# Optimization experiments

Measured on AMD Instinct MI355X. Metric: run time of the kernel, lower is better.

The kernel has to match this reference:

```python
import jax, jax.numpy as jnp
import numpy as np

N_NODES = 50000
N_EDGES = 800000
D_IN = 128
D_HID = 128
D_OUT = 128


def setup_inputs() -> dict:
    key = jax.random.key(0)
    ks = jax.random.split(key, 12)
    features = jax.random.normal(ks[0], (N_NODES, D_IN), dtype=jnp.float32)
    src = jax.random.randint(ks[1], (N_EDGES,), 0, N_NODES, dtype=jnp.int32)
    dst = jax.random.randint(ks[2], (N_EDGES,), 0, N_NODES, dtype=jnp.int32)
    s_in = 1.0 / np.sqrt(D_IN)
    s_hid = 1.0 / np.sqrt(D_HID)
    W1 = jax.random.normal(ks[3], (D_IN, D_HID), dtype=jnp.float32) * s_in
    b1 = jnp.zeros((D_HID,), dtype=jnp.float32)
    W2 = jax.random.normal(ks[4], (D_HID, D_HID), dtype=jnp.float32) * s_hid
    b2 = jnp.zeros((D_HID,), dtype=jnp.float32)
    W3 = jax.random.normal(ks[5], (D_HID, D_OUT), dtype=jnp.float32) * s_hid
    b3 = jnp.zeros((D_OUT,), dtype=jnp.float32)
    policy_w = jax.random.normal(ks[6], (D_OUT, 1), dtype=jnp.float32) * s_hid
    policy_b = jnp.zeros((1,), dtype=jnp.float32)
    value_w = jax.random.normal(ks[7], (D_OUT, 1), dtype=jnp.float32) * s_hid
    value_b = jnp.zeros((1,), dtype=jnp.float32)
    return {
        "features": features, "src": src, "dst": dst,
        "W1": W1, "b1": b1, "W2": W2, "b2": b2, "W3": W3, "b3": b3,
        "policy_w": policy_w, "policy_b": policy_b,
        "value_w": value_w, "value_b": value_b,
    }


def _graph_conv(h, src, dst, deg_inv, W, b, act):
    # DGL GraphConv with norm='left': scale source features by 1/out_degree,
    # sum messages over incoming edges, then linear transform + bias (+ act).
    hn = h * deg_inv  # [N, d]
    agg = jax.ops.segment_sum(hn[src], dst, num_segments=N_NODES)  # SpMM: [N, d]
    out = agg @ W + b
    return jax.nn.relu(out) if act else out


def reference(features, src, dst, W1, b1, W2, b2, W3, b3,
              policy_w, policy_b, value_w, value_b):
    ones = jnp.ones((src.shape[0],), dtype=features.dtype)
    deg = jax.ops.segment_sum(ones, src, num_segments=N_NODES)  # out-degree
    deg_inv = (1.0 / jnp.clip(deg, 1.0))[:, None]  # [N, 1]

    h = _graph_conv(features, src, dst, deg_inv, W1, b1, act=True)
    h = _graph_conv(h, src, dst, deg_inv, W2, b2, act=True)
    h = _graph_conv(h, src, dst, deg_inv, W3, b3, act=False)  # last layer: no activation

    mN = jnp.mean(h, axis=0, keepdims=True)  # mean readout over nodes, [1, D_OUT]
    PI = h @ policy_w + policy_b  # [N, 1]
    V = mN @ value_w + value_b    # [1, 1]
    return PI, V
```

## Files before the change

kernel.cpp:

```cpp
#include <hip/hip_runtime.h>


#define N_NODES 50000
#define N_EDGES 800000
#define D 128
#define NSH 8
#define PROWS (N_NODES + 8)
#define PANEL ((size_t)PROWS * 16)
#define NC 64
#define CSZ (N_EDGES / NC)
#define NW (N_NODES / 2)
#define CS_CAP (N_EDGES + 8 * N_NODES)


__global__ __launch_bounds__(512) void k_hist3(const int* __restrict__ src, const int* __restrict__ dst,
                                               unsigned* __restrict__ ghd16, unsigned* __restrict__ ghs16) {
    __shared__ unsigned h[NW];
    const int arr = blockIdx.x & 1;
    const int c   = blockIdx.x >> 1;
    const int t = threadIdx.x;
    for (int i = t; i < NW; i += 512) h[i] = 0u;
    __syncthreads();
    const int* __restrict__ col = arr ? src : dst;
    const int e0 = c * CSZ, e1 = e0 + CSZ;
    for (int e = e0 + t; e < e1; e += 512) {
        int n = col[e];
        atomicAdd(&h[n >> 1], 1u << ((n & 1) << 4));
    }
    __syncthreads();
    unsigned* __restrict__ outp = (arr ? ghs16 : ghd16) + (size_t)c * NW;
    for (int i = t; i < NW; i += 512) outp[i] = h[i];
}

__global__ __launch_bounds__(256) void k_merge3(unsigned* __restrict__ ghd16, const unsigned* __restrict__ ghs16,
                                                int* __restrict__ rowcnt, int* __restrict__ rowtrue,
                                                float* __restrict__ dinv) {
    int w = blockIdx.x * 256 + threadIdx.x;
    if (w >= NW) return;
    unsigned runlo = 0, runhi = 0;
#pragma unroll
    for (int c = 0; c < NC; c++) {
        unsigned v = ghd16[(size_t)c * NW + w];
        ghd16[(size_t)c * NW + w] = runlo | (runhi << 16);
        runlo += v & 0xffffu; runhi += v >> 16;
    }
    rowtrue[2 * w]     = (int)runlo;
    rowtrue[2 * w + 1] = (int)runhi;
    rowcnt[2 * w]      = (int)((runlo + 7u) & ~7u);
    rowcnt[2 * w + 1]  = (int)((runhi + 7u) & ~7u);
    unsigned dlo = 0, dhi = 0;
#pragma unroll
    for (int c = 0; c < NC; c++) {
        unsigned v = ghs16[(size_t)c * NW + w];
        dlo += v & 0xffffu; dhi += v >> 16;
    }
    dinv[2 * w]     = 1.0f / (float)(dlo > 1u ? dlo : 1u);
    dinv[2 * w + 1] = 1.0f / (float)(dhi > 1u ? dhi : 1u);
}

__global__ __launch_bounds__(1024) void k_scan1(const int* __restrict__ cnt, int* __restrict__ excl,
                                                int* __restrict__ blocksum, int n) {
    __shared__ int wsum[16];
    int i = blockIdx.x * 1024 + threadIdx.x;
    int v = (i < n) ? cnt[i] : 0;
    int lane = threadIdx.x & 63, wid = threadIdx.x >> 6;
    int x = v;
#pragma unroll
    for (int off = 1; off < 64; off <<= 1) {
        int y = __shfl_up(x, off, 64);
        if (lane >= off) x += y;
    }
    if (lane == 63) wsum[wid] = x;
    __syncthreads();
    if (threadIdx.x == 0) {
        int run = 0;
        for (int w = 0; w < 16; w++) { int t = wsum[w]; wsum[w] = run; run += t; }
        blocksum[blockIdx.x] = run;
    }
    __syncthreads();
    if (i < n) excl[i] = (x - v) + wsum[wid];
}

__global__ void k_scan2(const int* __restrict__ blocksum, int* __restrict__ blockoff,
                        int* __restrict__ rowptr_last, int nblk) {
    if (threadIdx.x == 0) {
        int run = 0;
        for (int b = 0; b < nblk; b++) { int t = blocksum[b]; blockoff[b] = run; run += t; }
        rowptr_last[0] = run;
    }
}

__global__ __launch_bounds__(1024) void k_scan3(int* __restrict__ excl, const int* __restrict__ blockoff, int n) {
    int i = blockIdx.x * 1024 + threadIdx.x;
    if (i < n) excl[i] += blockoff[blockIdx.x];
}

__global__ __launch_bounds__(512) void k_fill3(const int* __restrict__ src, const int* __restrict__ dst,
                                               const int* __restrict__ rowptr, const unsigned* __restrict__ ghd16,
                                               unsigned short* __restrict__ cs16) {
    __shared__ unsigned cnt[NW];
    const int c = blockIdx.x;
    const int t = threadIdx.x;
    for (int i = t; i < NW; i += 512) cnt[i] = 0u;
    __syncthreads();
    const unsigned* __restrict__ basep = ghd16 + (size_t)c * NW;
    const int e0 = c * CSZ, e1 = e0 + CSZ;
    for (int e = e0 + t; e < e1; e += 512) {
        int d = dst[e];
        int sh = (d & 1) << 4;
        unsigned old = atomicAdd(&cnt[d >> 1], 1u << sh);
        int p = (int)((old >> sh) & 0xffffu);
        int base = (int)((basep[d >> 1] >> sh) & 0xffffu);
        cs16[rowptr[d] + base + p] = (unsigned short)src[e];
    }
}

__global__ __launch_bounds__(256) void k_pad(const int* __restrict__ rowptr, const int* __restrict__ rowtrue,
                                             unsigned short* __restrict__ cs16,
                                             float* __restrict__ bufA, float* __restrict__ bufB) {
    int n = blockIdx.x * 256 + threadIdx.x;
    if (n < N_NODES) {
        int e0 = rowptr[n] + rowtrue[n], e1 = rowptr[n + 1];
        for (int e = e0; e < e1; e++) cs16[e] = (unsigned short)N_NODES;
    }
    if (blockIdx.x == 0) {
        int t = threadIdx.x;
        float* b = (t & 128) ? bufB : bufA;
        int p = (t >> 4) & 7, cc = t & 15;
        b[(size_t)p * PANEL + (size_t)N_NODES * 16 + cc] = 0.f;
    }
}


__global__ __launch_bounds__(256) void k_panelize(const float* __restrict__ in, const float* __restrict__ dinv,
                                                  float* __restrict__ outp) {
    int tid = blockIdx.x * 256 + threadIdx.x;
    if (tid >= N_NODES * 32) return;
    int p = tid / (N_NODES * 4);
    int r = tid - p * (N_NODES * 4);
    int node = r >> 2, qq = r & 3;
    float w = dinv[node];
    float4 v = *reinterpret_cast<const float4*>(&in[(size_t)node * D + p * 16 + qq * 4]);
    v.x *= w; v.y *= w; v.z *= w; v.w *= w;
    *reinterpret_cast<float4*>(&outp[(size_t)p * PANEL + (size_t)node * 16 + qq * 4]) = v;
}


__global__ __launch_bounds__(256) void k_agg(const float* __restrict__ hp,
                                             const int* __restrict__ rp, const unsigned short* __restrict__ cs16,
                                             float* __restrict__ outp) {
    const int l4 = threadIdx.x & 3;
    const int grp = threadIdx.x >> 2;
    const int slice = blockIdx.x & (NSH - 1);
    const int node = (blockIdx.x >> 3) * 64 + grp;
    if (node >= N_NODES) return;
    const float* __restrict__ pan = hp + (size_t)slice * PANEL + l4 * 4;
    int s0 = rp[node], s1 = rp[node + 1];
    float4 acc = {0.f, 0.f, 0.f, 0.f};
    for (int e = s0; e < s1; e += 8) {
        int4 r = *reinterpret_cast<const int4*>(&cs16[e]);
        int i0 = r.x & 0xffff, i1 = (r.x >> 16) & 0xffff;
        int i2 = r.y & 0xffff, i3 = (r.y >> 16) & 0xffff;
        int i4 = r.z & 0xffff, i5 = (r.z >> 16) & 0xffff;
        int i6 = r.w & 0xffff, i7 = (r.w >> 16) & 0xffff;
        float4 a0 = *reinterpret_cast<const float4*>(&pan[(size_t)i0 * 16]);
        float4 a1 = *reinterpret_cast<const float4*>(&pan[(size_t)i1 * 16]);
        float4 a2 = *reinterpret_cast<const float4*>(&pan[(size_t)i2 * 16]);
        float4 a3 = *reinterpret_cast<const float4*>(&pan[(size_t)i3 * 16]);
        float4 a4 = *reinterpret_cast<const float4*>(&pan[(size_t)i4 * 16]);
        float4 a5 = *reinterpret_cast<const float4*>(&pan[(size_t)i5 * 16]);
        float4 a6 = *reinterpret_cast<const float4*>(&pan[(size_t)i6 * 16]);
        float4 a7 = *reinterpret_cast<const float4*>(&pan[(size_t)i7 * 16]);
        acc.x += ((a0.x + a1.x) + (a2.x + a3.x)) + ((a4.x + a5.x) + (a6.x + a7.x));
        acc.y += ((a0.y + a1.y) + (a2.y + a3.y)) + ((a4.y + a5.y) + (a6.y + a7.y));
        acc.z += ((a0.z + a1.z) + (a2.z + a3.z)) + ((a4.z + a5.z) + (a6.z + a7.z));
        acc.w += ((a0.w + a1.w) + (a2.w + a3.w)) + ((a4.w + a5.w) + (a6.w + a7.w));
    }
    *reinterpret_cast<float4*>(&outp[(size_t)slice * PANEL + (size_t)node * 16 + l4 * 4]) = acc;
}


__global__ __launch_bounds__(256) void k_gemm(const float* __restrict__ in, const float* __restrict__ W,
                                              const float* __restrict__ bias, float* __restrict__ out,
                                              int nrows, int relu,
                                              const float* __restrict__ dscale,
                                              const float* __restrict__ pw, const float* __restrict__ pb,
                                              float* __restrict__ pi_out, float* __restrict__ colsum) {
    __shared__ float wl[D * D];
    __shared__ float at[64 * 64];
    int t = threadIdx.x;
    const int head = (pw != nullptr);
    for (int i = t; i < D * D / 4; i += 256)
        reinterpret_cast<float4*>(wl)[i] = reinterpret_cast<const float4*>(W)[i];
    const int tx = t & 15;
    const int ro = t >> 4;
    const int sr = t & 63;
    const int sq = t >> 6;
    float4 bv1 = reinterpret_cast<const float4*>(bias)[tx];
    float4 bv2 = reinterpret_cast<const float4*>(bias)[16 + tx];
    float4 pw1 = head ? reinterpret_cast<const float4*>(pw)[tx]      : float4{0, 0, 0, 0};
    float4 pw2 = head ? reinterpret_cast<const float4*>(pw)[16 + tx] : float4{0, 0, 0, 0};
    float pb0 = head ? pb[0] : 0.f;
    float4 cs1 = {0, 0, 0, 0}, cs2 = {0, 0, 0, 0};
    int ntiles = (nrows + 63) / 64;

#define LOADA(va, r0, h)                                                              \
    {                                                                                 \
        int gr_ = (r0) + sr;                                                          \
        if (gr_ < nrows) {                                                            \
            const float4* ap_ = reinterpret_cast<const float4*>(                      \
                &in[(size_t)((h) * 4 + sq) * PANEL + (size_t)gr_ * 16]);              \
            va[0] = ap_[0]; va[1] = ap_[1]; va[2] = ap_[2]; va[3] = ap_[3];           \
        } else {                                                                      \
            va[0] = va[1] = va[2] = va[3] = float4{0, 0, 0, 0};                       \
        }                                                                             \
    }

#define WRITEA(va)                                                                    \
    _Pragma("unroll")                                                                 \
    for (int q = 0; q < 4; q++) {                                                     \
        int kk_ = sq * 16 + q * 4;                                                    \
        at[(kk_ + 0) * 64 + sr] = va[q].x; at[(kk_ + 1) * 64 + sr] = va[q].y;         \
        at[(kk_ + 2) * 64 + sr] = va[q].z; at[(kk_ + 3) * 64 + sr] = va[q].w;         \
    }

#define KLOOP(H)                                                                      \
    {                                                                                 \
        const float* __restrict__ wlh = wl + (H) * 64 * D;                            \
        _Pragma("unroll 8")                                                           \
        for (int kk = 0; kk < 64; kk++) {                                             \
            float4 a  = *reinterpret_cast<const float4*>(&at[kk * 64 + ro * 4]);      \
            float4 w1 = *reinterpret_cast<const float4*>(&wlh[kk * D + tx * 4]);      \
            float4 w2 = *reinterpret_cast<const float4*>(&wlh[kk * D + 64 + tx * 4]); \
            acc[0][0] += a.x * w1.x; acc[0][1] += a.x * w1.y; acc[0][2] += a.x * w1.z; acc[0][3] += a.x * w1.w; \
            acc[0][4] += a.x * w2.x; acc[0][5] += a.x * w2.y; acc[0][6] += a.x * w2.z; acc[0][7] += a.x * w2.w; \
            acc[1][0] += a.y * w1.x; acc[1][1] += a.y * w1.y; acc[1][2] += a.y * w1.z; acc[1][3] += a.y * w1.w; \
            acc[1][4] += a.y * w2.x; acc[1][5] += a.y * w2.y; acc[1][6] += a.y * w2.z; acc[1][7] += a.y * w2.w; \
            acc[2][0] += a.z * w1.x; acc[2][1] += a.z * w1.y; acc[2][2] += a.z * w1.z; acc[2][3] += a.z * w1.w; \
            acc[2][4] += a.z * w2.x; acc[2][5] += a.z * w2.y; acc[2][6] += a.z * w2.z; acc[2][7] += a.z * w2.w; \
            acc[3][0] += a.w * w1.x; acc[3][1] += a.w * w1.y; acc[3][2] += a.w * w1.z; acc[3][3] += a.w * w1.w; \
            acc[3][4] += a.w * w2.x; acc[3][5] += a.w * w2.y; acc[3][6] += a.w * w2.z; acc[3][7] += a.w * w2.w; \
        }                                                                             \
    }

    float4 vaA[4], vaB[4];
    int tile0 = blockIdx.x;
    if (tile0 < ntiles) LOADA(vaA, tile0 * 64, 0);

    for (int tile = tile0; tile < ntiles; tile += gridDim.x) {
        int row0 = tile * 64;
        float acc[4][8];
#pragma unroll
        for (int j = 0; j < 4; j++)
#pragma unroll
            for (int c = 0; c < 8; c++) acc[j][c] = 0.f;

        __syncthreads();
        WRITEA(vaA);
        LOADA(vaB, row0, 1);
        __syncthreads();
        KLOOP(0);
        __syncthreads();
        WRITEA(vaB);
        {
            int nt = tile + gridDim.x;
            if (nt < ntiles) LOADA(vaA, nt * 64, 0);
        }
        __syncthreads();
        KLOOP(1);

#pragma unroll
        for (int j = 0; j < 4; j++) {
            int gr = row0 + ro * 4 + j;
            if (gr < nrows) {
                float4 o1, o2;
                o1.x = acc[j][0] + bv1.x; o1.y = acc[j][1] + bv1.y;
                o1.z = acc[j][2] + bv1.z; o1.w = acc[j][3] + bv1.w;
                o2.x = acc[j][4] + bv2.x; o2.y = acc[j][5] + bv2.y;
                o2.z = acc[j][6] + bv2.z; o2.w = acc[j][7] + bv2.w;
                if (relu) {
                    o1.x = fmaxf(o1.x, 0.f); o1.y = fmaxf(o1.y, 0.f);
                    o1.z = fmaxf(o1.z, 0.f); o1.w = fmaxf(o1.w, 0.f);
                    o2.x = fmaxf(o2.x, 0.f); o2.y = fmaxf(o2.y, 0.f);
                    o2.z = fmaxf(o2.z, 0.f); o2.w = fmaxf(o2.w, 0.f);
                }
                if (head) {
                    cs1.x += o1.x; cs1.y += o1.y; cs1.z += o1.z; cs1.w += o1.w;
                    cs2.x += o2.x; cs2.y += o2.y; cs2.z += o2.z; cs2.w += o2.w;
                    float pr = o1.x * pw1.x + o1.y * pw1.y + o1.z * pw1.z + o1.w * pw1.w
                             + o2.x * pw2.x + o2.y * pw2.y + o2.z * pw2.z + o2.w * pw2.w;
#pragma unroll
                    for (int m = 8; m > 0; m >>= 1) pr += __shfl_xor(pr, m, 16);
                    if (tx == 0) pi_out[gr] = pr + pb0;
                } else {
                    if (dscale) {
                        float w = dscale[gr];
                        o1.x *= w; o1.y *= w; o1.z *= w; o1.w *= w;
                        o2.x *= w; o2.y *= w; o2.z *= w; o2.w *= w;
                    }
                    size_t base1 = (size_t)(tx >> 2) * PANEL + (size_t)gr * 16 + (tx & 3) * 4;
                    *reinterpret_cast<float4*>(&out[base1]) = o1;
                    *reinterpret_cast<float4*>(&out[base1 + 4 * PANEL]) = o2;
                }
            }
        }
    }

    if (head) {
        __syncthreads();
        float* csl = at;
        if (t < D) csl[t] = 0.f;
        __syncthreads();
        atomicAdd(&csl[tx * 4 + 0], cs1.x);
        atomicAdd(&csl[tx * 4 + 1], cs1.y);
        atomicAdd(&csl[tx * 4 + 2], cs1.z);
        atomicAdd(&csl[tx * 4 + 3], cs1.w);
        atomicAdd(&csl[64 + tx * 4 + 0], cs2.x);
        atomicAdd(&csl[64 + tx * 4 + 1], cs2.y);
        atomicAdd(&csl[64 + tx * 4 + 2], cs2.z);
        atomicAdd(&csl[64 + tx * 4 + 3], cs2.w);
        __syncthreads();
        if (t < D) atomicAdd(&colsum[t], csl[t]);
    }
#undef LOADA
#undef WRITEA
#undef KLOOP
}


__global__ __launch_bounds__(128) void k_value(const float* __restrict__ colsum, const float* __restrict__ vw,
                                               const float* __restrict__ vb, float* __restrict__ out) {
    __shared__ float red[128];
    int t = threadIdx.x;
    red[t] = (colsum[t] * (1.0f / (float)N_NODES)) * vw[t];
    __syncthreads();
    for (int s = 64; s > 0; s >>= 1) {
        if (t < s) red[t] += red[t + s];
        __syncthreads();
    }
    if (t == 0) out[0] = red[0] + vb[0];
}

__global__ __launch_bounds__(64) void k_ws_too_small(float* __restrict__ out, int n) {
    int i = blockIdx.x * 64 + threadIdx.x;
    if (i < n) out[i] = -1e30f;
}


extern "C" void kernel_launch(void* const* d_in, const int* in_sizes, int n_in,
                              void* d_out, int out_size, void* d_ws, size_t ws_size,
                              hipStream_t stream) {
    const float* features = (const float*)d_in[0];
    const int*   src      = (const int*)d_in[1];
    const int*   dst      = (const int*)d_in[2];
    const float* W1 = (const float*)d_in[3];
    const float* b1 = (const float*)d_in[4];
    const float* W2 = (const float*)d_in[5];
    const float* b2 = (const float*)d_in[6];
    const float* W3 = (const float*)d_in[7];
    const float* b3 = (const float*)d_in[8];
    const float* pw = (const float*)d_in[9];
    const float* pb = (const float*)d_in[10];
    const float* vw = (const float*)d_in[11];
    const float* vb = (const float*)d_in[12];
    float* out = (float*)d_out;

    char* ws = (char*)d_ws;
    size_t off = 0;
    auto alloc = [&](size_t bytes) -> char* {
        char* p = ws + off;
        off += (bytes + 255) & ~(size_t)255;
        return p;
    };
    float* dinv     = (float*)alloc((size_t)N_NODES * 4);
    int*   rowptr   = (int*)alloc((size_t)(N_NODES + 1) * 4);
    int*   rowcnt   = (int*)alloc((size_t)N_NODES * 4);
    int*   rowtrue  = (int*)alloc((size_t)N_NODES * 4);
    int*   blocksum = (int*)alloc(64 * 4);
    int*   blockoff = (int*)alloc(64 * 4);
    float* colsum   = (float*)alloc(D * 4);
    unsigned short* cs16 = (unsigned short*)alloc((size_t)CS_CAP * 2);
    float* bufA     = (float*)alloc((size_t)NSH * PANEL * 4);
    float* bufB     = (float*)alloc((size_t)NSH * PANEL * 4);

    unsigned* ghd16 = (unsigned*)bufB;
    unsigned* ghs16 = ghd16 + (size_t)NC * NW;

    if (off > ws_size) {
        k_ws_too_small<<<(out_size + 63) / 64, 64, 0, stream>>>(out, out_size);
        return;
    }

    hipMemsetAsync(colsum, 0, (size_t)D * 4, stream);

    k_hist3<<<2 * NC, 512, 0, stream>>>(src, dst, ghd16, ghs16);
    k_merge3<<<(NW + 255) / 256, 256, 0, stream>>>(ghd16, ghs16, rowcnt, rowtrue, dinv);

    int nblk = (N_NODES + 1023) / 1024;
    k_scan1<<<nblk, 1024, 0, stream>>>(rowcnt, rowptr, blocksum, N_NODES);
    k_scan2<<<1, 64, 0, stream>>>(blocksum, blockoff, rowptr + N_NODES, nblk);
    k_scan3<<<nblk, 1024, 0, stream>>>(rowptr, blockoff, N_NODES);
    k_fill3<<<NC, 512, 0, stream>>>(src, dst, rowptr, ghd16, cs16);
    k_pad<<<(N_NODES + 255) / 256, 256, 0, stream>>>(rowptr, rowtrue, cs16, bufA, bufB);

    k_panelize<<<(N_NODES * 32 + 255) / 256, 256, 0, stream>>>(features, dinv, bufA);

    int aggblocks = ((N_NODES + 63) / 64) * NSH;
    k_agg<<<aggblocks, 256, 0, stream>>>(bufA, rowptr, cs16, bufB);
    k_gemm<<<512, 256, 0, stream>>>(bufB, W1, b1, bufB, N_NODES, 1, dinv,
                                    nullptr, nullptr, nullptr, nullptr);
    k_agg<<<aggblocks, 256, 0, stream>>>(bufB, rowptr, cs16, bufA);
    k_gemm<<<512, 256, 0, stream>>>(bufA, W2, b2, bufA, N_NODES, 1, dinv,
                                    nullptr, nullptr, nullptr, nullptr);
    k_agg<<<aggblocks, 256, 0, stream>>>(bufA, rowptr, cs16, bufB);
    k_gemm<<<512, 256, 0, stream>>>(bufB, W3, b3, nullptr, N_NODES, 0, nullptr,
                                    pw, pb, out, colsum);

    k_value<<<1, 128, 0, stream>>>(colsum, vw, vb, out + N_NODES);
}
```

Before: 321.6 us.

## Restructure GEMM to one 80-row tile per block with half-W staging

The GEMM kernel no longer loops persistently over 64-row tiles with the full 128x128 weight matrix in LDS. Each block now handles one 80-row tile (625 blocks), staging only half of W at a time in a smaller LDS buffer, which allows three blocks per CU via launch bounds. Each thread accumulates 5 rows instead of 4. The bounds checks are dropped because N_NODES divides evenly by 80. The goal is higher occupancy and less per-block LDS, at the cost of reloading W in every block and stalling on W staging between the two K halves.

```diff
diff --git a/kernel.cpp b/kernel.cpp
--- a/kernel.cpp
+++ b/kernel.cpp
@@ -11,6 +11,7 @@
 #define CSZ (N_EDGES / NC)
 #define NW (N_NODES / 2)
 #define CS_CAP (N_EDGES + 8 * N_NODES)
+#define TROWS 80
 
 
 __global__ __launch_bounds__(512) void k_hist3(const int* __restrict__ src, const int* __restrict__ dst,
@@ -180,129 +181,132 @@
 }
 
 
-__global__ __launch_bounds__(256) void k_gemm(const float* __restrict__ in, const float* __restrict__ W,
-                                              const float* __restrict__ bias, float* __restrict__ out,
-                                              int nrows, int relu,
-                                              const float* __restrict__ dscale,
-                                              const float* __restrict__ pw, const float* __restrict__ pb,
-                                              float* __restrict__ pi_out, float* __restrict__ colsum) {
-    __shared__ float wl[D * D];
-    __shared__ float at[64 * 64];
+__global__ __launch_bounds__(256, 3) void k_gemm(const float* __restrict__ in, const float* __restrict__ W,
+                                                 const float* __restrict__ bias, float* __restrict__ out,
+                                                 int nrows, int relu,
+                                                 const float* __restrict__ dscale,
+                                                 const float* __restrict__ pw, const float* __restrict__ pb,
+                                                 float* __restrict__ pi_out, float* __restrict__ colsum) {
+    __shared__ float wl[64 * D];
+    __shared__ float at[64 * TROWS];
     int t = threadIdx.x;
     const int head = (pw != nullptr);
-    for (int i = t; i < D * D / 4; i += 256)
-        reinterpret_cast<float4*>(wl)[i] = reinterpret_cast<const float4*>(W)[i];
     const int tx = t & 15;
     const int ro = t >> 4;
-    const int sr = t & 63;
-    const int sq = t >> 6;
+    const int row0 = blockIdx.x * TROWS;
     float4 bv1 = reinterpret_cast<const float4*>(bias)[tx];
     float4 bv2 = reinterpret_cast<const float4*>(bias)[16 + tx];
     float4 pw1 = head ? reinterpret_cast<const float4*>(pw)[tx]      : float4{0, 0, 0, 0};
     float4 pw2 = head ? reinterpret_cast<const float4*>(pw)[16 + tx] : float4{0, 0, 0, 0};
     float pb0 = head ? pb[0] : 0.f;
     float4 cs1 = {0, 0, 0, 0}, cs2 = {0, 0, 0, 0};
-    int ntiles = (nrows + 63) / 64;
-
-#define LOADA(va, r0, h)                                                              \
-    {                                                                                 \
-        int gr_ = (r0) + sr;                                                          \
-        if (gr_ < nrows) {                                                            \
-            const float4* ap_ = reinterpret_cast<const float4*>(                      \
-                &in[(size_t)((h) * 4 + sq) * PANEL + (size_t)gr_ * 16]);              \
-            va[0] = ap_[0]; va[1] = ap_[1]; va[2] = ap_[2]; va[3] = ap_[3];           \
-        } else {                                                                      \
-            va[0] = va[1] = va[2] = va[3] = float4{0, 0, 0, 0};                       \
-        }                                                                             \
-    }
-
-#define WRITEA(va)                                                                    \
-    _Pragma("unroll")                                                                 \
-    for (int q = 0; q < 4; q++) {                                                     \
-        int kk_ = sq * 16 + q * 4;                                                    \
-        at[(kk_ + 0) * 64 + sr] = va[q].x; at[(kk_ + 1) * 64 + sr] = va[q].y;         \
-        at[(kk_ + 2) * 64 + sr] = va[q].z; at[(kk_ + 3) * 64 + sr] = va[q].w;         \
-    }
-
-#define KLOOP(H)                                                                      \
-    {                                                                                 \
-        const float* __restrict__ wlh = wl + (H) * 64 * D;                            \
-        _Pragma("unroll 8")                                                           \
-        for (int kk = 0; kk < 64; kk++) {                                             \
-            float4 a  = *reinterpret_cast<const float4*>(&at[kk * 64 + ro * 4]);      \
-            float4 w1 = *reinterpret_cast<const float4*>(&wlh[kk * D + tx * 4]);      \
-            float4 w2 = *reinterpret_cast<const float4*>(&wlh[kk * D + 64 + tx * 4]); \
-            acc[0][0] += a.x * w1.x; acc[0][1] += a.x * w1.y; acc[0][2] += a.x * w1.z; acc[0][3] += a.x * w1.w; \
-            acc[0][4] += a.x * w2.x; acc[0][5] += a.x * w2.y; acc[0][6] += a.x * w2.z; acc[0][7] += a.x * w2.w; \
-            acc[1][0] += a.y * w1.x; acc[1][1] += a.y * w1.y; acc[1][2] += a.y * w1.z; acc[1][3] += a.y * w1.w; \
-            acc[1][4] += a.y * w2.x; acc[1][5] += a.y * w2.y; acc[1][6] += a.y * w2.z; acc[1][7] += a.y * w2.w; \
-            acc[2][0] += a.z * w1.x; acc[2][1] += a.z * w1.y; acc[2][2] += a.z * w1.z; acc[2][3] += a.z * w1.w; \
-            acc[2][4] += a.z * w2.x; acc[2][5] += a.z * w2.y; acc[2][6] += a.z * w2.z; acc[2][7] += a.z * w2.w; \
-            acc[3][0] += a.w * w1.x; acc[3][1] += a.w * w1.y; acc[3][2] += a.w * w1.z; acc[3][3] += a.w * w1.w; \
-            acc[3][4] += a.w * w2.x; acc[3][5] += a.w * w2.y; acc[3][6] += a.w * w2.z; acc[3][7] += a.w * w2.w; \
-        }                                                                             \
-    }
-
-    float4 vaA[4], vaB[4];
-    int tile0 = blockIdx.x;
-    if (tile0 < ntiles) LOADA(vaA, tile0 * 64, 0);
-
-    for (int tile = tile0; tile < ntiles; tile += gridDim.x) {
-        int row0 = tile * 64;
-        float acc[4][8];
-#pragma unroll
-        for (int j = 0; j < 4; j++)
-#pragma unroll
-            for (int c = 0; c < 8; c++) acc[j][c] = 0.f;
-
-        __syncthreads();
-        WRITEA(vaA);
-        LOADA(vaB, row0, 1);
-        __syncthreads();
-        KLOOP(0);
-        __syncthreads();
-        WRITEA(vaB);
-        {
-            int nt = tile + gridDim.x;
-            if (nt < ntiles) LOADA(vaA, nt * 64, 0);
+
+    int sidx[5], skb[5];
+#pragma unroll
+    for (int j = 0; j < 5; j++) {
+        int i = t + j * 256;
+        int r = i % TROWS;
+        int pq = i / TROWS;
+        sidx[j] = r;
+        skb[j] = (pq & 3) * 4 + (pq >> 2) * 16;
+    }
+
+#define LOADA(va, h)                                                                   \
+    _Pragma("unroll")                                                                  \
+    for (int j = 0; j < 5; j++) {                                                      \
+        int i = t + j * 256;                                                           \
+        int pq = i / TROWS;                                                            \
+        int p = (h) * 4 + (pq >> 2);                                                   \
+        int c4 = pq & 3;                                                               \
+        va[j] = *reinterpret_cast<const float4*>(                                      \
+            &in[(size_t)p * PANEL + (size_t)(row0 + sidx[j]) * 16 + c4 * 4]);          \
+    }
+
+#define WRITEA(va)                                                                     \
+    _Pragma("unroll")                                                                  \
+    for (int j = 0; j < 5; j++) {                                                      \
+        int kb = skb[j], r = sidx[j];                                                  \
+        at[(kb + 0) * TROWS + r] = va[j].x; at[(kb + 1) * TROWS + r] = va[j].y;        \
+        at[(kb + 2) * TROWS + r] = va[j].z; at[(kb + 3) * TROWS + r] = va[j].w;        \
+    }
+
+#define STAGEW(h)                                                                      \
+    _Pragma("unroll")                                                                  \
+    for (int j = 0; j < 8; j++) {                                                      \
+        int i = t + j * 256;                                                           \
+        reinterpret_cast<float4*>(wl)[i] =                                             \
+            reinterpret_cast<const float4*>(W + (h) * 64 * D)[i];                      \
+    }
+
+#define KLOOP                                                                          \
+    _Pragma("unroll 4")                                                                \
+    for (int kk = 0; kk < 64; kk++) {                                                  \
+        float4 a  = *reinterpret_cast<const float4*>(&at[kk * TROWS + ro * 5]);        \
+        float  a4 = at[kk * TROWS + ro * 5 + 4];                                       \
+        float4 w1 = *reinterpret_cast<const float4*>(&wl[kk * D + tx * 4]);            \
+        float4 w2 = *reinterpret_cast<const float4*>(&wl[kk * D + 64 + tx * 4]);       \
+        acc[0][0] += a.x * w1.x; acc[0][1] += a.x * w1.y; acc[0][2] += a.x * w1.z; acc[0][3] += a.x * w1.w; \
+        acc[0][4] += a.x * w2.x; acc[0][5] += a.x * w2.y; acc[0][6] += a.x * w2.z; acc[0][7] += a.x * w2.w; \
+        acc[1][0] += a.y * w1.x; acc[1][1] += a.y * w1.y; acc[1][2] += a.y * w1.z; acc[1][3] += a.y * w1.w; \
+        acc[1][4] += a.y * w2.x; acc[1][5] += a.y * w2.y; acc[1][6] += a.y * w2.z; acc[1][7] += a.y * w2.w; \
+        acc[2][0] += a.z * w1.x; acc[2][1] += a.z * w1.y; acc[2][2] += a.z * w1.z; acc[2][3] += a.z * w1.w; \
+        acc[2][4] += a.z * w2.x; acc[2][5] += a.z * w2.y; acc[2][6] += a.z * w2.z; acc[2][7] += a.z * w2.w; \
+        acc[3][0] += a.w * w1.x; acc[3][1] += a.w * w1.y; acc[3][2] += a.w * w1.z; acc[3][3] += a.w * w1.w; \
+        acc[3][4] += a.w * w2.x; acc[3][5] += a.w * w2.y; acc[3][6] += a.w * w2.z; acc[3][7] += a.w * w2.w; \
+        acc[4][0] += a4 * w1.x; acc[4][1] += a4 * w1.y; acc[4][2] += a4 * w1.z; acc[4][3] += a4 * w1.w;     \
+        acc[4][4] += a4 * w2.x; acc[4][5] += a4 * w2.y; acc[4][6] += a4 * w2.z; acc[4][7] += a4 * w2.w;     \
+    }
+
+    float acc[5][8];
+#pragma unroll
+    for (int j = 0; j < 5; j++)
+#pragma unroll
+        for (int c = 0; c < 8; c++) acc[j][c] = 0.f;
+
+    float4 va[5];
+    LOADA(va, 0);
+    STAGEW(0);
+    WRITEA(va);
+    __syncthreads();
+    LOADA(va, 1);
+    KLOOP;
+    __syncthreads();
+    WRITEA(va);
+    STAGEW(1);
+    __syncthreads();
+    KLOOP;
+
+#pragma unroll
+    for (int j = 0; j < 5; j++) {
+        int gr = row0 + ro * 5 + j;
+        float4 o1, o2;
+        o1.x = acc[j][0] + bv1.x; o1.y = acc[j][1] + bv1.y;
+        o1.z = acc[j][2] + bv1.z; o1.w = acc[j][3] + bv1.w;
+        o2.x = acc[j][4] + bv2.x; o2.y = acc[j][5] + bv2.y;
+        o2.z = acc[j][6] + bv2.z; o2.w = acc[j][7] + bv2.w;
+        if (relu) {
+            o1.x = fmaxf(o1.x, 0.f); o1.y = fmaxf(o1.y, 0.f);
+            o1.z = fmaxf(o1.z, 0.f); o1.w = fmaxf(o1.w, 0.f);
+            o2.x = fmaxf(o2.x, 0.f); o2.y = fmaxf(o2.y, 0.f);
+            o2.z = fmaxf(o2.z, 0.f); o2.w = fmaxf(o2.w, 0.f);
         }
-        __syncthreads();
-        KLOOP(1);
-
-#pragma unroll
-        for (int j = 0; j < 4; j++) {
-            int gr = row0 + ro * 4 + j;
-            if (gr < nrows) {
-                float4 o1, o2;
-                o1.x = acc[j][0] + bv1.x; o1.y = acc[j][1] + bv1.y;
-                o1.z = acc[j][2] + bv1.z; o1.w = acc[j][3] + bv1.w;
-                o2.x = acc[j][4] + bv2.x; o2.y = acc[j][5] + bv2.y;
-                o2.z = acc[j][6] + bv2.z; o2.w = acc[j][7] + bv2.w;
-                if (relu) {
-                    o1.x = fmaxf(o1.x, 0.f); o1.y = fmaxf(o1.y, 0.f);
-                    o1.z = fmaxf(o1.z, 0.f); o1.w = fmaxf(o1.w, 0.f);
-                    o2.x = fmaxf(o2.x, 0.f); o2.y = fmaxf(o2.y, 0.f);
-                    o2.z = fmaxf(o2.z, 0.f); o2.w = fmaxf(o2.w, 0.f);
-                }
-                if (head) {
-                    cs1.x += o1.x; cs1.y += o1.y; cs1.z += o1.z; cs1.w += o1.w;
-                    cs2.x += o2.x; cs2.y += o2.y; cs2.z += o2.z; cs2.w += o2.w;
-                    float pr = o1.x * pw1.x + o1.y * pw1.y + o1.z * pw1.z + o1.w * pw1.w
-                             + o2.x * pw2.x + o2.y * pw2.y + o2.z * pw2.z + o2.w * pw2.w;
-#pragma unroll
-                    for (int m = 8; m > 0; m >>= 1) pr += __shfl_xor(pr, m, 16);
-                    if (tx == 0) pi_out[gr] = pr + pb0;
-                } else {
-                    if (dscale) {
-                        float w = dscale[gr];
-                        o1.x *= w; o1.y *= w; o1.z *= w; o1.w *= w;
-                        o2.x *= w; o2.y *= w; o2.z *= w; o2.w *= w;
-                    }
-                    size_t base1 = (size_t)(tx >> 2) * PANEL + (size_t)gr * 16 + (tx & 3) * 4;
-                    *reinterpret_cast<float4*>(&out[base1]) = o1;
-                    *reinterpret_cast<float4*>(&out[base1 + 4 * PANEL]) = o2;
-                }
+        if (head) {
+            cs1.x += o1.x; cs1.y += o1.y; cs1.z += o1.z; cs1.w += o1.w;
+            cs2.x += o2.x; cs2.y += o2.y; cs2.z += o2.z; cs2.w += o2.w;
+            float pr = o1.x * pw1.x + o1.y * pw1.y + o1.z * pw1.z + o1.w * pw1.w
+                     + o2.x * pw2.x + o2.y * pw2.y + o2.z * pw2.z + o2.w * pw2.w;
+#pragma unroll
+            for (int m = 8; m > 0; m >>= 1) pr += __shfl_xor(pr, m, 16);
+            if (tx == 0) pi_out[gr] = pr + pb0;
+        } else {
+            if (dscale) {
+                float w = dscale[gr];
+                o1.x *= w; o1.y *= w; o1.z *= w; o1.w *= w;
+                o2.x *= w; o2.y *= w; o2.z *= w; o2.w *= w;
             }
+            size_t base1 = (size_t)(tx >> 2) * PANEL + (size_t)gr * 16 + (tx & 3) * 4;
+            *reinterpret_cast<float4*>(&out[base1]) = o1;
+            *reinterpret_cast<float4*>(&out[base1 + 4 * PANEL]) = o2;
         }
     }
 
@@ -324,6 +328,7 @@
     }
 #undef LOADA
 #undef WRITEA
+#undef STAGEW
 #undef KLOOP
 }
 
@@ -406,15 +411,16 @@
     k_panelize<<<(N_NODES * 32 + 255) / 256, 256, 0, stream>>>(features, dinv, bufA);
 
     int aggblocks = ((N_NODES + 63) / 64) * NSH;
+    int gemmblocks = N_NODES / TROWS;
     k_agg<<<aggblocks, 256, 0, stream>>>(bufA, rowptr, cs16, bufB);
-    k_gemm<<<512, 256, 0, stream>>>(bufB, W1, b1, bufB, N_NODES, 1, dinv,
-                                    nullptr, nullptr, nullptr, nullptr);
+    k_gemm<<<gemmblocks, 256, 0, stream>>>(bufB, W1, b1, bufB, N_NODES, 1, dinv,
+                                           nullptr, nullptr, nullptr, nullptr);
     k_agg<<<aggblocks, 256, 0, stream>>>(bufB, rowptr, cs16, bufA);
-    k_gemm<<<512, 256, 0, stream>>>(bufA, W2, b2, bufA, N_NODES, 1, dinv,
-                                    nullptr, nullptr, nullptr, nullptr);
+    k_gemm<<<gemmblocks, 256, 0, stream>>>(bufA, W2, b2, bufA, N_NODES, 1, dinv,
+                                           nullptr, nullptr, nullptr, nullptr);
     k_agg<<<aggblocks, 256, 0, stream>>>(bufA, rowptr, cs16, bufB);
-    k_gemm<<<512, 256, 0, stream>>>(bufB, W3, b3, nullptr, N_NODES, 0, nullptr,
-                                    pw, pb, out, colsum);
+    k_gemm<<<gemmblocks, 256, 0, stream>>>(bufB, W3, b3, nullptr, N_NODES, 0, nullptr,
+                                           pw, pb, out, colsum);
 
     k_value<<<1, 128, 0, stream>>>(colsum, vw, vb, out + N_NODES);
 }
```

After: 305.3 us. 5.1% less time.
